# Performance work log

Measured on AMD Instinct MI355X. Metric: run time of the kernel, lower is better.

Reference implementation:

```python
import jax, jax.numpy as jnp
import numpy as np

B, NQ, NK = 8, 1024, 1024
DQ = DK = DV = 512
H = 8
DS = DV // H
EPS = 1e-4
MAX_ITER = 3
SQRT_V = DV ** 0.25  # sqrt(sqrt(dim_V))


def setup_inputs() -> dict:
    key = jax.random.key(0)
    ks = jax.random.split(key, 8)
    s = 0.02
    return {
        "Q": jax.random.normal(ks[0], (B, NQ, DQ), jnp.float32),
        "K": jax.random.normal(ks[1], (B, NK, DK), jnp.float32),
        "Wq": jax.random.normal(ks[2], (DV, DQ), jnp.float32) * s,
        "bq": jnp.zeros((DV,), jnp.float32),
        "Wk": jax.random.normal(ks[3], (DV, DK), jnp.float32) * s,
        "bk": jnp.zeros((DV,), jnp.float32),
        "Wv": jax.random.normal(ks[4], (DV, DK), jnp.float32) * s,
        "bv": jnp.zeros((DV,), jnp.float32),
        "Wo": jax.random.normal(ks[5], (DV, DV), jnp.float32) * s,
        "bo": jnp.zeros((DV,), jnp.float32),
    }


def _split_heads(x):
    # torch.cat(x.split(ds, 2), 0): head-major stacking along batch
    b, n, _ = x.shape
    return x.reshape(b, n, H, DS).transpose(2, 0, 1, 3).reshape(H * b, n, DS)


def _merge_heads(x, b):
    # torch.cat(x.split(b, 0), 2): inverse of _split_heads
    _, n, ds = x.shape
    return x.reshape(H, b, n, ds).transpose(1, 2, 0, 3).reshape(b, n, H * ds)


def _sinkhorn_plan(x, y):
    # x: [M, P1, d], y: [M, P2, d]; cost = pairwise Euclidean (p=2) distance.
    x2 = jnp.sum(x * x, axis=-1)[:, :, None]
    y2 = jnp.sum(y * y, axis=-1)[:, None, :]
    C = jnp.sqrt(jnp.maximum(x2 + y2 - 2.0 * jnp.einsum("mid,mjd->mij", x, y), 0.0))
    m, p1, p2 = C.shape
    log_a = -jnp.log(jnp.float32(p1))  # uniform marginals
    log_b = -jnp.log(jnp.float32(p2))
    u = jnp.zeros((m, p1), C.dtype)
    v = jnp.zeros((m, p2), C.dtype)
    for _ in range(MAX_ITER):  # fixed small iteration count (max_iter=3)
        u = EPS * (log_a - jax.scipy.special.logsumexp((v[:, None, :] - C) / EPS, axis=2))
        v = EPS * (log_b - jax.scipy.special.logsumexp((u[:, :, None] - C) / EPS, axis=1))
    # transport plan P: [M, P1, P2]
    return jnp.exp((u[:, :, None] + v[:, None, :] - C) / EPS)


def reference(Q, K, Wq, bq, Wk, bk, Wv, bv, Wo, bo):
    q = Q @ Wq.T + bq            # [B, NQ, DV]
    k = K @ Wk.T + bk            # [B, NK, DV]
    v = K @ Wv.T + bv            # [B, NK, DV]
    b = Q.shape[0]
    q_, k_, v_ = _split_heads(q), _split_heads(k), _split_heads(v)  # [H*B, N, DS]
    A = _sinkhorn_plan(q_ / SQRT_V, k_ / SQRT_V)                    # [H*B, NQ, NK]
    O = _merge_heads(q_ + jnp.einsum("mij,mjd->mid", A, v_), b)     # [B, NQ, DV]
    return O + jax.nn.relu(O @ Wo.T + bo)
```

## Files before the change

kernel.cpp:

```cpp
#include <hip/hip_runtime.h>
#include <hip/hip_bf16.h>
#include <math.h>

#define NB 8
#define NN 1024
#define ND 512
#define NH 8
#define NDS 64
#define NM 64
#define LOG_A (-6.93147180559945f)
#define SQRT_V 4.75682846001088f
#define INV_SQRT_V 0.210224103813429f
#define INV_EPS 10000.0f
#define L2E  1.44269504088896f
#define LN2F 0.693147180559945f
#define IEL2 14426.9504088896f

#define SPLIT_ELEMS ((size_t)NM * NN * NDS)
#define W_ELEMS     ((size_t)ND * ND)
#define UV_FLOATS   ((size_t)NM * NN)

typedef unsigned short u16;
typedef unsigned int   u32;
typedef __attribute__((ext_vector_type(8))) short bf16x8;
typedef __attribute__((ext_vector_type(4))) float f32x4;

#define MFMA16(a,b,c) __builtin_amdgcn_mfma_f32_16x16x32_bf16(a,b,c,0,0,0)

__device__ __forceinline__ u16 f2bf_t(float x) {
  return (u16)(__float_as_uint(x) >> 16);
}
__device__ __forceinline__ float bf2f(u16 h) {
  return __uint_as_float(((u32)h) << 16);
}
__device__ __forceinline__ float fast_sqrt(float x) {
  float r;
  asm("v_sqrt_f32 %0, %1" : "=v"(r) : "v"(x));
  return r;
}
__device__ __forceinline__ float fast_exp2(float x) {
  float r;
  asm("v_exp_f32 %0, %1" : "=v"(r) : "v"(x));
  return r;
}
__device__ __forceinline__ float max3f(float a, float b, float c) {
  float r;
  asm("v_max3_f32 %0, %1, %2, %3" : "=v"(r) : "v"(a), "v"(b), "v"(c));
  return r;
}

__global__ __launch_bounds__(256) void k_split(
    const float* __restrict__ X, u16* __restrict__ hi, u16* __restrict__ lo)
{
  const size_t i = ((size_t)blockIdx.x * 256 + threadIdx.x) * 4;
  float4 v = *(const float4*)&X[i];
  const float* vp = (const float*)&v;
  u16 h[4], l[4];
#pragma unroll
  for (int j = 0; j < 4; ++j) {
    h[j] = f2bf_t(vp[j]);
    l[j] = f2bf_t(vp[j] - bf2f(h[j]));
  }
  uint2 ph, pl;
  ph.x = (u32)h[0] | ((u32)h[1] << 16);
  ph.y = (u32)h[2] | ((u32)h[3] << 16);
  pl.x = (u32)l[0] | ((u32)l[1] << 16);
  pl.y = (u32)l[2] | ((u32)l[3] << 16);
  *(uint2*)&hi[i] = ph;
  *(uint2*)&lo[i] = pl;
}

__global__ __launch_bounds__(256) void k_proj_mfma(
    const u16* __restrict__ Xh, const u16* __restrict__ Xl,
    const u16* __restrict__ Wh, const u16* __restrict__ Wl,
    const float* __restrict__ bias, u16* __restrict__ oh,
    u16* __restrict__ ol, u16* __restrict__ oT,
    float* __restrict__ nrm, float scale, int mode)
{
  __shared__ __align__(16) u16 Xhs[64][72];
  __shared__ __align__(16) u16 Xls[64][72];
  __shared__ __align__(16) u16 Whs[64][72];
  __shared__ __align__(16) u16 Wls[64][72];
  const int t = threadIdx.x;
  const int r0 = blockIdx.x * 64;
  const int h  = blockIdx.y;
  const int c0 = h * 64;
  const int w = t >> 6, l = t & 63;
  const int c = l & 15, kg = l >> 4;
  const int srow = t >> 2;
  const int skoff = (t & 3) * 16;

  f32x4 acc[4];
#pragma unroll
  for (int cf = 0; cf < 4; ++cf) acc[cf] = (f32x4){0.f, 0.f, 0.f, 0.f};

  for (int kt = 0; kt < 8; ++kt) {
    const int k0 = kt * 64;
    __syncthreads();
    {
      const u16* gxh = &Xh[(size_t)(r0 + srow) * ND + k0 + skoff];
      const u16* gxl = &Xl[(size_t)(r0 + srow) * ND + k0 + skoff];
      const u16* gwh = &Wh[(size_t)(c0 + srow) * ND + k0 + skoff];
      const u16* gwl = &Wl[(size_t)(c0 + srow) * ND + k0 + skoff];
      *(bf16x8*)&Xhs[srow][skoff]     = *(const bf16x8*)gxh;
      *(bf16x8*)&Xhs[srow][skoff + 8] = *(const bf16x8*)(gxh + 8);
      *(bf16x8*)&Xls[srow][skoff]     = *(const bf16x8*)gxl;
      *(bf16x8*)&Xls[srow][skoff + 8] = *(const bf16x8*)(gxl + 8);
      *(bf16x8*)&Whs[srow][skoff]     = *(const bf16x8*)gwh;
      *(bf16x8*)&Whs[srow][skoff + 8] = *(const bf16x8*)(gwh + 8);
      *(bf16x8*)&Wls[srow][skoff]     = *(const bf16x8*)gwl;
      *(bf16x8*)&Wls[srow][skoff + 8] = *(const bf16x8*)(gwl + 8);
    }
    __syncthreads();
#pragma unroll
    for (int ks = 0; ks < 2; ++ks) {
      bf16x8 Ah = *(const bf16x8*)&Xhs[w * 16 + c][ks * 32 + kg * 8];
      bf16x8 Al = *(const bf16x8*)&Xls[w * 16 + c][ks * 32 + kg * 8];
#pragma unroll
      for (int cf = 0; cf < 4; ++cf) {
        bf16x8 Bh = *(const bf16x8*)&Whs[cf * 16 + c][ks * 32 + kg * 8];
        bf16x8 Bl = *(const bf16x8*)&Wls[cf * 16 + c][ks * 32 + kg * 8];
        acc[cf] = MFMA16(Ah, Bh, acc[cf]);
        acc[cf] = MFMA16(Ah, Bl, acc[cf]);
        acc[cf] = MFMA16(Al, Bh, acc[cf]);
      }
    }
  }

  const int bb = r0 >> 10;
  const int n0 = r0 & 1023;
  const size_t mrow = (size_t)(h * NB + bb) * NN;
  if (mode == 0) {
    float ns[4] = {0.f, 0.f, 0.f, 0.f};
#pragma unroll
    for (int cf = 0; cf < 4; ++cf) {
      const int col = c0 + cf * 16 + c;
      const float bv = bias[col];
#pragma unroll
      for (int r = 0; r < 4; ++r) {
        float v = (acc[cf][r] + bv) * scale;
        u16 hv = f2bf_t(v);
        u16 lv = f2bf_t(v - bf2f(hv));
        ns[r] = fmaf(v, v, ns[r]);
        int n = n0 + w * 16 + kg * 4 + r;
        size_t idx = (mrow + n) * NDS + cf * 16 + c;
        oh[idx] = hv;
        ol[idx] = lv;
      }
    }
#pragma unroll
    for (int off = 1; off <= 8; off <<= 1)
#pragma unroll
      for (int r = 0; r < 4; ++r) ns[r] += __shfl_xor(ns[r], off);
    if (c == 0) {
#pragma unroll
      for (int r = 0; r < 4; ++r)
        nrm[mrow + n0 + w * 16 + kg * 4 + r] = ns[r];
    }
  } else {
#pragma unroll
    for (int cf = 0; cf < 4; ++cf) {
      const int d = cf * 16 + c;
      const float bv = bias[c0 + d];
      u16 p0 = f2bf_t((acc[cf][0] + bv) * scale);
      u16 p1 = f2bf_t((acc[cf][1] + bv) * scale);
      u16 p2 = f2bf_t((acc[cf][2] + bv) * scale);
      u16 p3 = f2bf_t((acc[cf][3] + bv) * scale);
      uint2 p;
      p.x = (u32)p0 | ((u32)p1 << 16);
      p.y = (u32)p2 | ((u32)p3 << 16);
      *(uint2*)&oT[((size_t)(h * NB + bb) * NDS + d) * NN + n0 + w * 16 + kg * 4] = p;
    }
  }
}

__global__ __launch_bounds__(512, 4) void k_lse_mfma(
    const u16* __restrict__ Ah_, const u16* __restrict__ Al_,
    const u16* __restrict__ Bh_, const u16* __restrict__ Bl_,
    const float* __restrict__ Anrm, const float* __restrict__ Bnrm,
    const float* __restrict__ din, float* __restrict__ dout, int first)
{
  __shared__ __align__(16) float din_s[NN];
  __shared__ __align__(16) float y2_s[NN];
  __shared__ __align__(16) u16 Bhs[2][64][72];
  __shared__ __align__(16) u16 Bls[2][64][72];
  const int t = threadIdx.x;
  const int Lb = blockIdx.x;
  const int xcd = Lb & 7, slot = Lb >> 3;
  const int m = xcd + 8 * (slot >> 3);
  const int a0 = (slot & 7) * 128;

  if (first) {
    *(float2*)&din_s[t * 2] = make_float2(0.f, 0.f);
  } else {
    float2 dv = *(const float2*)&din[(size_t)m * NN + t * 2];
    dv.x *= L2E; dv.y *= L2E;
    *(float2*)&din_s[t * 2] = dv;
  }
  *(float2*)&y2_s[t * 2] = *(const float2*)&Bnrm[(size_t)m * NN + t * 2];

  const int w = t >> 6, l = t & 63;
  const int c = l & 15, kg = l >> 4;
  const int arow = a0 + w * 16;
  const size_t mbase = (size_t)m * NN * NDS;

  const u16* pah = &Ah_[mbase + (size_t)(arow + c) * NDS + kg * 8];
  const u16* pal = &Al_[mbase + (size_t)(arow + c) * NDS + kg * 8];
  bf16x8 A0h = *(const bf16x8*)pah;
  bf16x8 A1h = *(const bf16x8*)(pah + 32);
  bf16x8 A0l = *(const bf16x8*)pal;
  bf16x8 A1l = *(const bf16x8*)(pal + 32);

  float x2r[4];
#pragma unroll
  for (int r = 0; r < 4; ++r) x2r[r] = Anrm[(size_t)m * NN + arow + kg * 4 + r];
  float M[4], S[4];
#pragma unroll
  for (int r = 0; r < 4; ++r) { M[r] = -3.0e38f; S[r] = 0.f; }

  const int srow = t >> 3;
  const int skoff = (t & 7) * 8;
  const u16* gh = &Bh_[mbase + (size_t)srow * NDS + skoff];
  const u16* gl = &Bl_[mbase + (size_t)srow * NDS + skoff];
  bf16x8 rh = *(const bf16x8*)gh;
  bf16x8 rl = *(const bf16x8*)gl;

  for (int bt = 0; bt < 16; ++bt) {
    const int b0 = bt * 64;
    const int buf = bt & 1;
    *(bf16x8*)&Bhs[buf][srow][skoff] = rh;
    *(bf16x8*)&Bls[buf][srow][skoff] = rl;
    {
      const size_t noff = (size_t)((bt + 1) & 15) * 4096;
      rh = *(const bf16x8*)(gh + noff);
      rl = *(const bf16x8*)(gl + noff);
    }
    __syncthreads();
    f32x4 acc[4];
#pragma unroll
    for (int cf = 0; cf < 4; ++cf) {
      const int bl = cf * 16 + c;
      bf16x8 B0h = *(const bf16x8*)&Bhs[buf][bl][kg * 8];
      bf16x8 B1h = *(const bf16x8*)&Bhs[buf][bl][kg * 8 + 32];
      bf16x8 B0l = *(const bf16x8*)&Bls[buf][bl][kg * 8];
      bf16x8 B1l = *(const bf16x8*)&Bls[buf][bl][kg * 8 + 32];
      f32x4 a = {0.f, 0.f, 0.f, 0.f};
      a = MFMA16(A0h, B0h, a);
      a = MFMA16(A0h, B0l, a);
      a = MFMA16(A0l, B0h, a);
      a = MFMA16(A1h, B1h, a);
      a = MFMA16(A1h, B1l, a);
      a = MFMA16(A1l, B1h, a);
      acc[cf] = a;
    }
    float X[4][4];
#pragma unroll
    for (int cf = 0; cf < 4; ++cf) {
      const int col = b0 + cf * 16 + c;
      const float vb2 = din_s[col];
      const float y2  = y2_s[col];
#pragma unroll
      for (int r = 0; r < 4; ++r) {
        float d2 = fmaf(-2.f, acc[cf][r], x2r[r] + y2);
        float sq = fast_sqrt(fmaxf(d2, 0.f));
        X[cf][r] = fmaf(-IEL2, sq, vb2);
      }
    }
#pragma unroll
    for (int r = 0; r < 4; ++r) {
      float m1 = max3f(X[0][r], X[1][r], X[2][r]);
      float nm = max3f(m1, X[3][r], M[r]);
      float s4 = fast_exp2(X[0][r] - nm) + fast_exp2(X[1][r] - nm)
               + fast_exp2(X[2][r] - nm) + fast_exp2(X[3][r] - nm);
      S[r] = fmaf(S[r], fast_exp2(M[r] - nm), s4);
      M[r] = nm;
    }
  }
#pragma unroll
  for (int off = 1; off <= 8; off <<= 1) {
#pragma unroll
    for (int r = 0; r < 4; ++r) {
      float Mo = __shfl_xor(M[r], off);
      float So = __shfl_xor(S[r], off);
      float nm = fmaxf(M[r], Mo);
      S[r] = S[r] * fast_exp2(M[r] - nm) + So * fast_exp2(Mo - nm);
      M[r] = nm;
    }
  }
  if (c == 0) {
#pragma unroll
    for (int r = 0; r < 4; ++r)
      dout[(size_t)m * NN + arow + kg * 4 + r] =
          LOG_A - M[r] * LN2F - __logf(S[r]);
  }
}

__global__ __launch_bounds__(512, 4) void k_pv_mfma(
    const u16* __restrict__ qh, const u16* __restrict__ ql,
    const u16* __restrict__ kh, const u16* __restrict__ kl,
    const u16* __restrict__ vT, const float* __restrict__ qn,
    const float* __restrict__ kn, const float* __restrict__ ue,
    const float* __restrict__ ve, u16* __restrict__ Oh_, u16* __restrict__ Ol_)
{
  __shared__ __align__(16) float ve_s[NN];
  __shared__ __align__(16) float y2_s[NN];
  __shared__ __align__(16) u16 Bhs[2][64][72];
  __shared__ __align__(16) u16 Bls[2][64][72];
  __shared__ __align__(16) u16 Vs[2][64][72];
  __shared__ __align__(16) u16 pT[8][16][40];
  const int t = threadIdx.x;
  const int Lb = blockIdx.x;
  const int xcd = Lb & 7, slot = Lb >> 3;
  const int m = xcd + 8 * (slot >> 3);
  const int a0 = (slot & 7) * 128;
  {
    float2 vv = *(const float2*)&ve[(size_t)m * NN + t * 2];
    vv.x *= L2E; vv.y *= L2E;
    *(float2*)&ve_s[t * 2] = vv;
  }
  *(float2*)&y2_s[t * 2] = *(const float2*)&kn[(size_t)m * NN + t * 2];

  const int w = t >> 6, l = t & 63;
  const int c = l & 15, kg = l >> 4;
  const int arow = a0 + w * 16;
  const size_t mbase = (size_t)m * NN * NDS;

  const u16* pah = &qh[mbase + (size_t)(arow + c) * NDS + kg * 8];
  const u16* pal = &ql[mbase + (size_t)(arow + c) * NDS + kg * 8];
  bf16x8 A0h = *(const bf16x8*)pah;
  bf16x8 A1h = *(const bf16x8*)(pah + 32);
  bf16x8 A0l = *(const bf16x8*)pal;
  bf16x8 A1l = *(const bf16x8*)(pal + 32);

  float x2r[4], uer2[4];
#pragma unroll
  for (int r = 0; r < 4; ++r) {
    x2r[r]  = qn[(size_t)m * NN + arow + kg * 4 + r];
    uer2[r] = ue[(size_t)m * NN + arow + kg * 4 + r] * L2E;
  }
  f32x4 pacc[4];
#pragma unroll
  for (int df = 0; df < 4; ++df) pacc[df] = (f32x4){0.f, 0.f, 0.f, 0.f};

  const int srow = t >> 3;
  const int skoff = (t & 7) * 8;
  const u16* gh = &kh[mbase + (size_t)srow * NDS + skoff];
  const u16* gl = &kl[mbase + (size_t)srow * NDS + skoff];
  const u16* gv = &vT[((size_t)m * NDS + srow) * NN + skoff];
  bf16x8 rh = *(const bf16x8*)gh;
  bf16x8 rl = *(const bf16x8*)gl;
  bf16x8 rv = *(const bf16x8*)gv;

  for (int bt = 0; bt < 16; ++bt) {
    const int b0 = bt * 64;
    const int buf = bt & 1;
    *(bf16x8*)&Bhs[buf][srow][skoff] = rh;
    *(bf16x8*)&Bls[buf][srow][skoff] = rl;
    *(bf16x8*)&Vs[buf][srow][skoff]  = rv;
    {
      const int nbt = (bt + 1) & 15;
      rh = *(const bf16x8*)(gh + (size_t)nbt * 4096);
      rl = *(const bf16x8*)(gl + (size_t)nbt * 4096);
      rv = *(const bf16x8*)(gv + (size_t)nbt * 64);
    }
    __syncthreads();
#pragma unroll
    for (int ph = 0; ph < 2; ++ph) {
      f32x4 acc[2];
#pragma unroll
      for (int q = 0; q < 2; ++q) {
        const int cf = ph * 2 + q;
        const int bl = cf * 16 + c;
        bf16x8 B0h = *(const bf16x8*)&Bhs[buf][bl][kg * 8];
        bf16x8 B1h = *(const bf16x8*)&Bhs[buf][bl][kg * 8 + 32];
        bf16x8 B0l = *(const bf16x8*)&Bls[buf][bl][kg * 8];
        bf16x8 B1l = *(const bf16x8*)&Bls[buf][bl][kg * 8 + 32];
        f32x4 a = {0.f, 0.f, 0.f, 0.f};
        a = MFMA16(A0h, B0h, a);
        a = MFMA16(A0h, B0l, a);
        a = MFMA16(A0l, B0h, a);
        a = MFMA16(A1h, B1h, a);
        a = MFMA16(A1h, B1l, a);
        a = MFMA16(A1l, B1h, a);
        acc[q] = a;
      }
#pragma unroll
      for (int q = 0; q < 2; ++q) {
        const int cf = ph * 2 + q;
        const int col = b0 + cf * 16 + c;
        const float ve2 = ve_s[col];
        const float y2  = y2_s[col];
#pragma unroll
        for (int r = 0; r < 4; ++r) {
          float d2 = fmaf(-2.f, acc[q][r], x2r[r] + y2);
          float sq = fast_sqrt(fmaxf(d2, 0.f));
          float p  = fast_exp2(fmaf(-IEL2, sq, uer2[r] + ve2));
          pT[w][kg * 4 + r][q * 16 + c] = f2bf_t(p);
        }
      }
      bf16x8 Pa = *(const bf16x8*)&pT[w][c][kg * 8];
#pragma unroll
      for (int df = 0; df < 4; ++df) {
        bf16x8 Vb = *(const bf16x8*)&Vs[buf][df * 16 + c][ph * 32 + kg * 8];
        pacc[df] = MFMA16(Pa, Vb, pacc[df]);
      }
    }
  }
#pragma unroll
  for (int df = 0; df < 4; ++df) {
#pragma unroll
    for (int r = 0; r < 4; ++r) {
      int row = arow + kg * 4 + r;
      int d = df * 16 + c;
      size_t qi = mbase + (size_t)row * NDS + d;
      float qv = bf2f(qh[qi]) + bf2f(ql[qi]);
      float o  = fmaf(SQRT_V, qv, pacc[df][r]);
      u16 hv = f2bf_t(o);
      Oh_[qi] = hv;
      Ol_[qi] = f2bf_t(o - bf2f(hv));
    }
  }
}

__global__ __launch_bounds__(256) void k_out_mfma(
    const u16* __restrict__ Oh_, const u16* __restrict__ Ol_,
    const u16* __restrict__ Wh, const u16* __restrict__ Wl,
    const float* __restrict__ bo, float* __restrict__ out)
{
  __shared__ __align__(16) u16 Ahs[64][72];
  __shared__ __align__(16) u16 Als[64][72];
  __shared__ __align__(16) u16 Whs[64][72];
  __shared__ __align__(16) u16 Wls[64][72];
  const int t = threadIdx.x;
  const int r0 = blockIdx.x * 64;
  const int c0 = blockIdx.y * 64;
  const int bb = r0 >> 10;
  const int n0 = r0 & 1023;
  const int w = t >> 6, l = t & 63;
  const int c = l & 15, kg = l >> 4;
  const int srow = t >> 2;
  const int skoff = (t & 3) * 16;

  f32x4 acc[4];
#pragma unroll
  for (int cf = 0; cf < 4; ++cf) acc[cf] = (f32x4){0.f, 0.f, 0.f, 0.f};

  for (int kt = 0; kt < 8; ++kt) {
    __syncthreads();
    {
      const size_t ob = ((size_t)(kt * NB + bb) * NN + n0 + srow) * NDS;
      const u16* gah = &Oh_[ob + skoff];
      const u16* gal = &Ol_[ob + skoff];
      const u16* gwh = &Wh[(size_t)(c0 + srow) * ND + kt * 64 + skoff];
      const u16* gwl = &Wl[(size_t)(c0 + srow) * ND + kt * 64 + skoff];
      *(bf16x8*)&Ahs[srow][skoff]     = *(const bf16x8*)gah;
      *(bf16x8*)&Ahs[srow][skoff + 8] = *(const bf16x8*)(gah + 8);
      *(bf16x8*)&Als[srow][skoff]     = *(const bf16x8*)gal;
      *(bf16x8*)&Als[srow][skoff + 8] = *(const bf16x8*)(gal + 8);
      *(bf16x8*)&Whs[srow][skoff]     = *(const bf16x8*)gwh;
      *(bf16x8*)&Whs[srow][skoff + 8] = *(const bf16x8*)(gwh + 8);
      *(bf16x8*)&Wls[srow][skoff]     = *(const bf16x8*)gwl;
      *(bf16x8*)&Wls[srow][skoff + 8] = *(const bf16x8*)(gwl + 8);
    }
    __syncthreads();
#pragma unroll
    for (int ks = 0; ks < 2; ++ks) {
      bf16x8 Ah = *(const bf16x8*)&Ahs[w * 16 + c][ks * 32 + kg * 8];
      bf16x8 Al = *(const bf16x8*)&Als[w * 16 + c][ks * 32 + kg * 8];
#pragma unroll
      for (int cf = 0; cf < 4; ++cf) {
        bf16x8 Bh = *(const bf16x8*)&Whs[cf * 16 + c][ks * 32 + kg * 8];
        bf16x8 Bl = *(const bf16x8*)&Wls[cf * 16 + c][ks * 32 + kg * 8];
        acc[cf] = MFMA16(Ah, Bh, acc[cf]);
        acc[cf] = MFMA16(Ah, Bl, acc[cf]);
        acc[cf] = MFMA16(Al, Bh, acc[cf]);
      }
    }
  }
#pragma unroll
  for (int cf = 0; cf < 4; ++cf) {
    const int col = c0 + cf * 16 + c;
    const int d = cf * 16 + c;
    const float bv = bo[col];
#pragma unroll
    for (int r = 0; r < 4; ++r) {
      const int n = n0 + w * 16 + kg * 4 + r;
      const size_t oi = ((size_t)(blockIdx.y * NB + bb) * NN + n) * NDS + d;
      float om = bf2f(Oh_[oi]) + bf2f(Ol_[oi]);
      out[(size_t)(r0 + w * 16 + kg * 4 + r) * ND + col] =
          om + fmaxf(acc[cf][r] + bv, 0.f);
    }
  }
}

extern "C" void kernel_launch(void* const* d_in, const int* in_sizes, int n_in,
                              void* d_out, int out_size, void* d_ws, size_t ws_size,
                              hipStream_t stream) {
  const float* Q  = (const float*)d_in[0];
  const float* K  = (const float*)d_in[1];
  const float* Wq = (const float*)d_in[2];
  const float* bq = (const float*)d_in[3];
  const float* Wk = (const float*)d_in[4];
  const float* bk = (const float*)d_in[5];
  const float* Wv = (const float*)d_in[6];
  const float* bv = (const float*)d_in[7];
  const float* Wo = (const float*)d_in[8];
  const float* bo = (const float*)d_in[9];
  float* out = (float*)d_out;

  const size_t need_bytes =
      7 * SPLIT_ELEMS * sizeof(u16) + 8 * W_ELEMS * sizeof(u16) +
      4 * UV_FLOATS * sizeof(float);
  if (ws_size < need_bytes) return;

  u16* qh = (u16*)d_ws;
  u16* ql = qh + SPLIT_ELEMS;
  u16* kh = ql + SPLIT_ELEMS;
  u16* kl = kh + SPLIT_ELEMS;
  u16* vT = kl + SPLIT_ELEMS;
  u16* Oh = vT + SPLIT_ELEMS;
  u16* Ol = Oh + SPLIT_ELEMS;
  u16* wqh = Ol + SPLIT_ELEMS;
  u16* wql = wqh + W_ELEMS;
  u16* wkh = wql + W_ELEMS;
  u16* wkl = wkh + W_ELEMS;
  u16* wvh = wkl + W_ELEMS;
  u16* wvl = wvh + W_ELEMS;
  u16* woh = wvl + W_ELEMS;
  u16* wol = woh + W_ELEMS;
  float* ue = (float*)(wol + W_ELEMS);
  float* ve = ue + UV_FLOATS;
  float* qn = ve + UV_FLOATS;
  float* kn = qn + UV_FLOATS;

  u16* Qrh = Oh;
  u16* Qrl = Ol;
  u16* Krh = (u16*)d_out;
  u16* Krl = Krh + SPLIT_ELEMS;

  dim3 blk(256);
  k_split<<<dim3(4096), blk, 0, stream>>>(Q, Qrh, Qrl);
  k_split<<<dim3(4096), blk, 0, stream>>>(K, Krh, Krl);
  k_split<<<dim3(256), blk, 0, stream>>>(Wq, wqh, wql);
  k_split<<<dim3(256), blk, 0, stream>>>(Wk, wkh, wkl);
  k_split<<<dim3(256), blk, 0, stream>>>(Wv, wvh, wvl);
  k_split<<<dim3(256), blk, 0, stream>>>(Wo, woh, wol);
  k_proj_mfma<<<dim3(128, 8), blk, 0, stream>>>(Qrh, Qrl, wqh, wql, bq, qh, ql, nullptr, qn, INV_SQRT_V, 0);
  k_proj_mfma<<<dim3(128, 8), blk, 0, stream>>>(Krh, Krl, wkh, wkl, bk, kh, kl, nullptr, kn, INV_SQRT_V, 0);
  k_proj_mfma<<<dim3(128, 8), blk, 0, stream>>>(Krh, Krl, wvh, wvl, bv, nullptr, nullptr, vT, nullptr, 1.0f, 1);
  for (int it = 0; it < 3; ++it) {
    k_lse_mfma<<<dim3(512), dim3(512), 0, stream>>>(qh, ql, kh, kl, qn, kn, ve, ue, it == 0 ? 1 : 0);
    k_lse_mfma<<<dim3(512), dim3(512), 0, stream>>>(kh, kl, qh, ql, kn, qn, ue, ve, 0);
  }
  k_pv_mfma<<<dim3(512), dim3(512), 0, stream>>>(qh, ql, kh, kl, vT, qn, kn, ue, ve, Oh, Ol);
  k_out_mfma<<<dim3(128, 8), blk, 0, stream>>>(Oh, Ol, woh, wol, bo, out);
}
```

Before: 373.2 us.

## Double-buffer projection GEMM tiles and replace syncthreads with LDS-only barriers

Measured after the change: 372.7 us. No clear change (-0.1%).

```diff
diff --git a/kernel.cpp b/kernel.cpp
--- a/kernel.cpp
+++ b/kernel.cpp
@@ -48,6 +48,13 @@
   asm("v_max3_f32 %0, %1, %2, %3" : "=v"(r) : "v"(a), "v"(b), "v"(c));
   return r;
 }
+__device__ __forceinline__ void soft_barrier() {
+  asm volatile("s_waitcnt lgkmcnt(0)" ::: "memory");
+  __builtin_amdgcn_sched_barrier(0);
+  __builtin_amdgcn_s_barrier();
+  __builtin_amdgcn_sched_barrier(0);
+  asm volatile("" ::: "memory");
+}
 
 __global__ __launch_bounds__(256) void k_split(
     const float* __restrict__ X, u16* __restrict__ hi, u16* __restrict__ lo)
@@ -70,17 +77,17 @@
   *(uint2*)&lo[i] = pl;
 }
 
-__global__ __launch_bounds__(256) void k_proj_mfma(
+__global__ __launch_bounds__(256, 2) void k_proj_mfma(
     const u16* __restrict__ Xh, const u16* __restrict__ Xl,
     const u16* __restrict__ Wh, const u16* __restrict__ Wl,
     const float* __restrict__ bias, u16* __restrict__ oh,
     u16* __restrict__ ol, u16* __restrict__ oT,
     float* __restrict__ nrm, float scale, int mode)
 {
-  __shared__ __align__(16) u16 Xhs[64][72];
-  __shared__ __align__(16) u16 Xls[64][72];
-  __shared__ __align__(16) u16 Whs[64][72];
-  __shared__ __align__(16) u16 Wls[64][72];
+  __shared__ __align__(16) u16 Xhs[2][64][72];
+  __shared__ __align__(16) u16 Xls[2][64][72];
+  __shared__ __align__(16) u16 Whs[2][64][72];
+  __shared__ __align__(16) u16 Wls[2][64][72];
   const int t = threadIdx.x;
   const int r0 = blockIdx.x * 64;
   const int h  = blockIdx.y;
@@ -90,36 +97,46 @@
   const int srow = t >> 2;
   const int skoff = (t & 3) * 16;
 
+  const u16* gxh = &Xh[(size_t)(r0 + srow) * ND + skoff];
+  const u16* gxl = &Xl[(size_t)(r0 + srow) * ND + skoff];
+  const u16* gwh = &Wh[(size_t)(c0 + srow) * ND + skoff];
+  const u16* gwl = &Wl[(size_t)(c0 + srow) * ND + skoff];
+
+  bf16x8 rxh0 = *(const bf16x8*)gxh, rxh1 = *(const bf16x8*)(gxh + 8);
+  bf16x8 rxl0 = *(const bf16x8*)gxl, rxl1 = *(const bf16x8*)(gxl + 8);
+  bf16x8 rwh0 = *(const bf16x8*)gwh, rwh1 = *(const bf16x8*)(gwh + 8);
+  bf16x8 rwl0 = *(const bf16x8*)gwl, rwl1 = *(const bf16x8*)(gwl + 8);
+
   f32x4 acc[4];
 #pragma unroll
   for (int cf = 0; cf < 4; ++cf) acc[cf] = (f32x4){0.f, 0.f, 0.f, 0.f};
 
   for (int kt = 0; kt < 8; ++kt) {
-    const int k0 = kt * 64;
-    __syncthreads();
+    const int buf = kt & 1;
+    *(bf16x8*)&Xhs[buf][srow][skoff]     = rxh0;
+    *(bf16x8*)&Xhs[buf][srow][skoff + 8] = rxh1;
+    *(bf16x8*)&Xls[buf][srow][skoff]     = rxl0;
+    *(bf16x8*)&Xls[buf][srow][skoff + 8] = rxl1;
+    *(bf16x8*)&Whs[buf][srow][skoff]     = rwh0;
+    *(bf16x8*)&Whs[buf][srow][skoff + 8] = rwh1;
+    *(bf16x8*)&Wls[buf][srow][skoff]     = rwl0;
+    *(bf16x8*)&Wls[buf][srow][skoff + 8] = rwl1;
     {
-      const u16* gxh = &Xh[(size_t)(r0 + srow) * ND + k0 + skoff];
-      const u16* gxl = &Xl[(size_t)(r0 + srow) * ND + k0 + skoff];
-      const u16* gwh = &Wh[(size_t)(c0 + srow) * ND + k0 + skoff];
-      const u16* gwl = &Wl[(size_t)(c0 + srow) * ND + k0 + skoff];
-      *(bf16x8*)&Xhs[srow][skoff]     = *(const bf16x8*)gxh;
-      *(bf16x8*)&Xhs[srow][skoff + 8] = *(const bf16x8*)(gxh + 8);
-      *(bf16x8*)&Xls[srow][skoff]     = *(const bf16x8*)gxl;
-      *(bf16x8*)&Xls[srow][skoff + 8] = *(const bf16x8*)(gxl + 8);
-      *(bf16x8*)&Whs[srow][skoff]     = *(const bf16x8*)gwh;
-      *(bf16x8*)&Whs[srow][skoff + 8] = *(const bf16x8*)(gwh + 8);
-      *(bf16x8*)&Wls[srow][skoff]     = *(const bf16x8*)gwl;
-      *(bf16x8*)&Wls[srow][skoff + 8] = *(const bf16x8*)(gwl + 8);
-    }
-    __syncthreads();
+      const int nk = ((kt + 1) & 7) * 64;
+      rxh0 = *(const bf16x8*)(gxh + nk); rxh1 = *(const bf16x8*)(gxh + nk + 8);
+      rxl0 = *(const bf16x8*)(gxl + nk); rxl1 = *(const bf16x8*)(gxl + nk + 8);
+      rwh0 = *(const bf16x8*)(gwh + nk); rwh1 = *(const bf16x8*)(gwh + nk + 8);
+      rwl0 = *(const bf16x8*)(gwl + nk); rwl1 = *(const bf16x8*)(gwl + nk + 8);
+    }
+    soft_barrier();
 #pragma unroll
     for (int ks = 0; ks < 2; ++ks) {
-      bf16x8 Ah = *(const bf16x8*)&Xhs[w * 16 + c][ks * 32 + kg * 8];
-      bf16x8 Al = *(const bf16x8*)&Xls[w * 16 + c][ks * 32 + kg * 8];
+      bf16x8 Ah = *(const bf16x8*)&Xhs[buf][w * 16 + c][ks * 32 + kg * 8];
+      bf16x8 Al = *(const bf16x8*)&Xls[buf][w * 16 + c][ks * 32 + kg * 8];
 #pragma unroll
       for (int cf = 0; cf < 4; ++cf) {
-        bf16x8 Bh = *(const bf16x8*)&Whs[cf * 16 + c][ks * 32 + kg * 8];
-        bf16x8 Bl = *(const bf16x8*)&Wls[cf * 16 + c][ks * 32 + kg * 8];
+        bf16x8 Bh = *(const bf16x8*)&Whs[buf][cf * 16 + c][ks * 32 + kg * 8];
+        bf16x8 Bl = *(const bf16x8*)&Wls[buf][cf * 16 + c][ks * 32 + kg * 8];
         acc[cf] = MFMA16(Ah, Bh, acc[cf]);
         acc[cf] = MFMA16(Ah, Bl, acc[cf]);
         acc[cf] = MFMA16(Al, Bh, acc[cf]);
@@ -224,6 +241,7 @@
   const u16* gl = &Bl_[mbase + (size_t)srow * NDS + skoff];
   bf16x8 rh = *(const bf16x8*)gh;
   bf16x8 rl = *(const bf16x8*)gl;
+  __syncthreads();
 
   for (int bt = 0; bt < 16; ++bt) {
     const int b0 = bt * 64;
@@ -235,7 +253,7 @@
       rh = *(const bf16x8*)(gh + noff);
       rl = *(const bf16x8*)(gl + noff);
     }
-    __syncthreads();
+    soft_barrier();
     f32x4 acc[4];
 #pragma unroll
     for (int cf = 0; cf < 4; ++cf) {
@@ -350,6 +368,7 @@
   bf16x8 rh = *(const bf16x8*)gh;
   bf16x8 rl = *(const bf16x8*)gl;
   bf16x8 rv = *(const bf16x8*)gv;
+  __syncthreads();
 
   for (int bt = 0; bt < 16; ++bt) {
     const int b0 = bt * 64;
@@ -363,7 +382,7 @@
       rl = *(const bf16x8*)(gl + (size_t)nbt * 4096);
       rv = *(const bf16x8*)(gv + (size_t)nbt * 64);
     }
-    __syncthreads();
+    soft_barrier();
 #pragma unroll
     for (int ph = 0; ph < 2; ++ph) {
       f32x4 acc[2];
@@ -422,15 +441,15 @@
   }
 }
 
-__global__ __launch_bounds__(256) void k_out_mfma(
+__global__ __launch_bounds__(256, 2) void k_out_mfma(
     const u16* __restrict__ Oh_, const u16* __restrict__ Ol_,
     const u16* __restrict__ Wh, const u16* __restrict__ Wl,
     const float* __restrict__ bo, float* __restrict__ out)
 {
-  __shared__ __align__(16) u16 Ahs[64][72];
-  __shared__ __align__(16) u16 Als[64][72];
-  __shared__ __align__(16) u16 Whs[64][72];
-  __shared__ __align__(16) u16 Wls[64][72];
+  __shared__ __align__(16) u16 Ahs[2][64][72];
+  __shared__ __align__(16) u16 Als[2][64][72];
+  __shared__ __align__(16) u16 Whs[2][64][72];
+  __shared__ __align__(16) u16 Wls[2][64][72];
   const int t = threadIdx.x;
   const int r0 = blockIdx.x * 64;
   const int c0 = blockIdx.y * 64;
@@ -445,32 +464,50 @@
 #pragma unroll
   for (int cf = 0; cf < 4; ++cf) acc[cf] = (f32x4){0.f, 0.f, 0.f, 0.f};
 
+  bf16x8 rah0, rah1, ral0, ral1, rwh0, rwh1, rwl0, rwl1;
+  {
+    const size_t ob = ((size_t)(0 * NB + bb) * NN + n0 + srow) * NDS;
+    const u16* gah = &Oh_[ob + skoff];
+    const u16* gal = &Ol_[ob + skoff];
+    const u16* gwh = &Wh[(size_t)(c0 + srow) * ND + skoff];
+    const u16* gwl = &Wl[(size_t)(c0 + srow) * ND + skoff];
+    rah0 = *(const bf16x8*)gah; rah1 = *(const bf16x8*)(gah + 8);
+    ral0 = *(const bf16x8*)gal; ral1 = *(const bf16x8*)(gal + 8);
+    rwh0 = *(const bf16x8*)gwh; rwh1 = *(const bf16x8*)(gwh + 8);
+    rwl0 = *(const bf16x8*)gwl; rwl1 = *(const bf16x8*)(gwl + 8);
+  }
+
   for (int kt = 0; kt < 8; ++kt) {
-    __syncthreads();
+    const int buf = kt & 1;
+    *(bf16x8*)&Ahs[buf][srow][skoff]     = rah0;
+    *(bf16x8*)&Ahs[buf][srow][skoff + 8] = rah1;
+    *(bf16x8*)&Als[buf][srow][skoff]     = ral0;
+    *(bf16x8*)&Als[buf][srow][skoff + 8] = ral1;
+    *(bf16x8*)&Whs[buf][srow][skoff]     = rwh0;
+    *(bf16x8*)&Whs[buf][srow][skoff + 8] = rwh1;
+    *(bf16x8*)&Wls[buf][srow][skoff]     = rwl0;
+    *(bf16x8*)&Wls[buf][srow][skoff + 8] = rwl1;
     {
-      const size_t ob = ((size_t)(kt * NB + bb) * NN + n0 + srow) * NDS;
+      const int nkt = (kt + 1) & 7;
+      const size_t ob = ((size_t)(nkt * NB + bb) * NN + n0 + srow) * NDS;
       const u16* gah = &Oh_[ob + skoff];
       const u16* gal = &Ol_[ob + skoff];
-      const u16* gwh = &Wh[(size_t)(c0 + srow) * ND + kt * 64 + skoff];
-      const u16* gwl = &Wl[(size_t)(c0 + srow) * ND + kt * 64 + skoff];
-      *(bf16x8*)&Ahs[srow][skoff]     = *(const bf16x8*)gah;
-      *(bf16x8*)&Ahs[srow][skoff + 8] = *(const bf16x8*)(gah + 8);
-      *(bf16x8*)&Als[srow][skoff]     = *(const bf16x8*)gal;
-      *(bf16x8*)&Als[srow][skoff + 8] = *(const bf16x8*)(gal + 8);
-      *(bf16x8*)&Whs[srow][skoff]     = *(const bf16x8*)gwh;
-      *(bf16x8*)&Whs[srow][skoff + 8] = *(const bf16x8*)(gwh + 8);
-      *(bf16x8*)&Wls[srow][skoff]     = *(const bf16x8*)gwl;
-      *(bf16x8*)&Wls[srow][skoff + 8] = *(const bf16x8*)(gwl + 8);
-    }
-    __syncthreads();
+      const u16* gwh = &Wh[(size_t)(c0 + srow) * ND + nkt * 64 + skoff];
+      const u16* gwl = &Wl[(size_t)(c0 + srow) * ND + nkt * 64 + skoff];
+      rah0 = *(const bf16x8*)gah; rah1 = *(const bf16x8*)(gah + 8);
+      ral0 = *(const bf16x8*)gal; ral1 = *(const bf16x8*)(gal + 8);
+      rwh0 = *(const bf16x8*)gwh; rwh1 = *(const bf16x8*)(gwh + 8);
+      rwl0 = *(const bf16x8*)gwl; rwl1 = *(const bf16x8*)(gwl + 8);
+    }
+    soft_barrier();
 #pragma unroll
     for (int ks = 0; ks < 2; ++ks) {
-      bf16x8 Ah = *(const bf16x8*)&Ahs[w * 16 + c][ks * 32 + kg * 8];
-      bf16x8 Al = *(const bf16x8*)&Als[w * 16 + c][ks * 32 + kg * 8];
+      bf16x8 Ah = *(const bf16x8*)&Ahs[buf][w * 16 + c][ks * 32 + kg * 8];
+      bf16x8 Al = *(const bf16x8*)&Als[buf][w * 16 + c][ks * 32 + kg * 8];
 #pragma unroll
       for (int cf = 0; cf < 4; ++cf) {
-        bf16x8 Bh = *(const bf16x8*)&Whs[cf * 16 + c][ks * 32 + kg * 8];
-        bf16x8 Bl = *(const bf16x8*)&Wls[cf * 16 + c][ks * 32 + kg * 8];
+        bf16x8 Bh = *(const bf16x8*)&Whs[buf][cf * 16 + c][ks * 32 + kg * 8];
+        bf16x8 Bl = *(const bf16x8*)&Wls[buf][cf * 16 + c][ks * 32 + kg * 8];
         acc[cf] = MFMA16(Ah, Bh, acc[cf]);
         acc[cf] = MFMA16(Ah, Bl, acc[cf]);
         acc[cf] = MFMA16(Al, Bh, acc[cf]);
```
